# Performance work log

Hardware: AMD Instinct MI355X
Metric: run time of the kernel (lower is better)

Reference implementation:

```python
import jax, jax.numpy as jnp
import numpy as np

M, K, N = 4096, 4096, 11008  # tokens, in_features, out_features


def setup_inputs() -> dict:
    key = jax.random.key(0)
    k1, k2, k3, k4 = jax.random.split(key, 4)
    x = jax.random.normal(k1, (M, K), dtype=jnp.float32)
    weight = jax.random.randint(k2, (N, K), -128, 128).astype(jnp.int8)
    # per-output-channel scale, small positive values as from real quantization
    weight_scale = (jax.random.uniform(k3, (N,), dtype=jnp.float32) * 0.01 + 1e-4)
    bias = jax.random.normal(k4, (N,), dtype=jnp.float32)
    return {"x": x, "weight": weight, "weight_scale": weight_scale, "bias": bias}


def reference(x, weight, weight_scale, bias):
    # Dynamic per-token symmetric quantization of activations to int8.
    x_scale = jnp.max(jnp.abs(x), axis=-1, keepdims=True) / 127.0  # [M, 1]
    x_scale = jnp.maximum(x_scale, 1e-8)
    x_q = jnp.clip(jnp.round(x / x_scale), -128, 127).astype(jnp.int8)  # [M, K]
    acc = jax.lax.dot_general(
        x_q, weight,
        dimension_numbers=(((1,), (1,)), ((), ())),
        preferred_element_type=jnp.int32,
    )
    # Dequantize: per-token activation scale * per-channel weight scale, add bias.
    out = acc.astype(jnp.float32) * x_scale * weight_scale[None, :] + bias[None, :]
    return out
```

## Files before the change

### kernel.cpp

```cpp
#include <hip/hip_runtime.h>
#include <stdint.h>

#define M_DIM 4096
#define K_DIM 4096
#define N_DIM 11008

typedef int v4i __attribute__((ext_vector_type(4)));

#define LDSP(p) ((__attribute__((address_space(3))) void*)(uintptr_t)(p))
#define GLBP(p) ((__attribute__((address_space(1))) void*)(uintptr_t)(p))

__global__ __launch_bounds__(256) void quant_rows(const float* __restrict__ x,
                                                  int8_t* __restrict__ xq,
                                                  float* __restrict__ xs_out) {
    const int row = blockIdx.x;
    const int t = threadIdx.x;
    const float4* xr = (const float4*)(x + (size_t)row * K_DIM);

    float4 v[4];
    float amax = 0.0f;
#pragma unroll
    for (int r = 0; r < 4; ++r) {
        v[r] = xr[t + r * 256];
        amax = fmaxf(amax, fmaxf(fmaxf(fabsf(v[r].x), fabsf(v[r].y)),
                                 fmaxf(fabsf(v[r].z), fabsf(v[r].w))));
    }
#pragma unroll
    for (int off = 32; off > 0; off >>= 1)
        amax = fmaxf(amax, __shfl_xor(amax, off));

    __shared__ float smax[4];
    if ((t & 63) == 0) smax[t >> 6] = amax;
    __syncthreads();
    amax = fmaxf(fmaxf(smax[0], smax[1]), fmaxf(smax[2], smax[3]));

    const float xs = fmaxf(amax / 127.0f, 1e-8f);
    if (t == 0) xs_out[row] = xs;

    int* qo = (int*)(xq + (size_t)row * K_DIM);
#pragma unroll
    for (int r = 0; r < 4; ++r) {
        int q0 = (int)rintf(v[r].x / xs);
        int q1 = (int)rintf(v[r].y / xs);
        int q2 = (int)rintf(v[r].z / xs);
        int q3 = (int)rintf(v[r].w / xs);
        q0 = min(127, max(-128, q0));
        q1 = min(127, max(-128, q1));
        q2 = min(127, max(-128, q2));
        q3 = min(127, max(-128, q3));
        int packed = (q0 & 255) | ((q1 & 255) << 8) | ((q2 & 255) << 16) | (q3 << 24);
        qo[t + r * 256] = packed;
    }
}

__global__ __launch_bounds__(256) void prep_weight(const void* __restrict__ wraw,
                                                   int8_t* __restrict__ w8) {
    const int* wi = (const int*)wraw;
    int c = 0;
#pragma unroll
    for (int i = 0; i < 64; ++i) {
        int w = wi[i];
        c += (w >= -128 && w <= 127) ? 1 : 0;
    }
    const size_t tid = (size_t)blockIdx.x * 256 + threadIdx.x;
    if (c >= 32) {
        union { int4 v; char b[16]; } o;
#pragma unroll
        for (int g = 0; g < 4; ++g) {
            int4 w = ((const int4*)wraw)[tid * 4 + g];
            o.b[g * 4 + 0] = (char)w.x;
            o.b[g * 4 + 1] = (char)w.y;
            o.b[g * 4 + 2] = (char)w.z;
            o.b[g * 4 + 3] = (char)w.w;
        }
        ((int4*)w8)[tid] = o.v;
    } else {
        ((int4*)w8)[tid] = ((const int4*)wraw)[tid];
    }
}

__global__ __launch_bounds__(512, 2) void w8a8_gemm(const int8_t* __restrict__ xq,
                                                    const float* __restrict__ xscale,
                                                    const int8_t* __restrict__ wgt,
                                                    const float* __restrict__ wscale,
                                                    const float* __restrict__ bias,
                                                    float* __restrict__ out) {
    __shared__ __align__(16) int8_t lds_a[3][32768];
    __shared__ __align__(16) int8_t lds_b[2][32768];

    const int t = threadIdx.x;
    const int lane = t & 63;
    const int wave = t >> 6;
    const int wm = wave >> 2;
    const int wn = wave & 3;
    const int quad = lane >> 4;
    const int l15 = lane & 15;

    const int wg = blockIdx.x;
    const int xcd = wg & 7;
    const int u = wg >> 3;
    const int bm = 2 * xcd + (u & 1);
    const int bn = u >> 1;

    const int8_t* pa = xq + (size_t)bm * 256 * K_DIM;
    const int8_t* pb = wgt + (size_t)bn * 256 * K_DIM;

    const int srow = t >> 3;
    const size_t soff = (size_t)srow * K_DIM + (size_t)(((t & 7) ^ (srow & 7)) << 4);
    const size_t g64 = (size_t)64 * K_DIM;

#define STAGE_TILE(gb, lb)                                                                   \
    do {                                                                                     \
        __builtin_amdgcn_global_load_lds(GLBP((gb) + soff), LDSP((lb) + t * 16), 16, 0, 0);  \
        __builtin_amdgcn_global_load_lds(GLBP((gb) + soff + g64), LDSP((lb) + 8192 + t * 16), 16, 0, 0); \
        __builtin_amdgcn_global_load_lds(GLBP((gb) + soff + 2 * g64), LDSP((lb) + 16384 + t * 16), 16, 0, 0); \
        __builtin_amdgcn_global_load_lds(GLBP((gb) + soff + 3 * g64), LDSP((lb) + 24576 + t * 16), 16, 0, 0); \
    } while (0)

    int abase[2], bbase[2];
#pragma unroll
    for (int ks = 0; ks < 2; ++ks) {
        const int ar = wm * 128 + l15;
        abase[ks] = ar * 128 + (((ks * 4 + quad) ^ (l15 & 7)) << 4);
        const int br = wn * 64 + l15;
        bbase[ks] = br * 128 + (((ks * 4 + quad) ^ (l15 & 7)) << 4);
    }

    v4i acc[8][4] = {};
    v4i af[8], bf[8];

#define READ_B8(SB)                                                   \
    _Pragma("unroll") for (int j = 0; j < 4; ++j) {                   \
        bf[j] = *(const v4i*)(&lds_b[SB][bbase[0] + j * 2048]);       \
        bf[4 + j] = *(const v4i*)(&lds_b[SB][bbase[1] + j * 2048]);   \
    }
#define READ_A8(SA, KS)                                               \
    _Pragma("unroll") for (int i = 0; i < 8; ++i)                     \
        af[i] = *(const v4i*)(&lds_a[SA][abase[KS] + i * 2048]);
#define MFMA16(B0)                                                    \
    _Pragma("unroll") for (int i = 0; i < 8; ++i)                     \
    _Pragma("unroll") for (int j = 0; j < 4; ++j)                     \
        acc[i][j] = __builtin_amdgcn_mfma_i32_16x16x64_i8(            \
            af[i], bf[(B0) + j], acc[i][j], 0, 0, 0);
#define PH_PRE                                                        \
    __builtin_amdgcn_s_barrier();                                     \
    asm volatile("s_waitcnt lgkmcnt(0)" ::: "memory");                \
    __builtin_amdgcn_s_setprio(1);
#define PH_POST                                                       \
    __builtin_amdgcn_s_setprio(0);                                    \
    __builtin_amdgcn_s_barrier();

    STAGE_TILE(pa, &lds_a[0][0]);
    STAGE_TILE(pb, &lds_b[0][0]);
    STAGE_TILE(pa + 128, &lds_a[1][0]);
    STAGE_TILE(pb + 128, &lds_b[1][0]);
    asm volatile("s_waitcnt vmcnt(8)" ::: "memory");
    __builtin_amdgcn_s_barrier();

#define DO_TILE(U)                                                       \
    {                                                                    \
        constexpr int SA = (U) % 3;                                      \
        constexpr int SB = (U) % 2;                                      \
        constexpr int SA2 = ((U) + 2) % 3;                               \
        const size_t k2 = (size_t)(t0 + (U) + 2) * 128;                  \
                                                                \
        READ_B8(SB);                                                     \
        READ_A8(SA, 0);                                                  \
        STAGE_TILE(pa + k2, &lds_a[SA2][0]);                             \
        PH_PRE; MFMA16(0); PH_POST;                                      \
                                                                \
        READ_A8(SA, 1);                                                  \
        STAGE_TILE(pb + k2, &lds_b[SB][0]);                              \
        asm volatile("s_waitcnt vmcnt(8)" ::: "memory");                 \
        PH_PRE; MFMA16(4); PH_POST;                                      \
    }

#pragma unroll 1
    for (int t0 = 0; t0 < 30; t0 += 6) {
        DO_TILE(0)
        DO_TILE(1)
        DO_TILE(2)
        DO_TILE(3)
        DO_TILE(4)
        DO_TILE(5)
    }
    READ_B8(0);
    READ_A8(0, 0);
    PH_PRE; MFMA16(0); PH_POST;
    READ_A8(0, 1);
    asm volatile("s_waitcnt vmcnt(0)" ::: "memory");
    PH_PRE; MFMA16(4); PH_POST;
    READ_B8(1);
    READ_A8(1, 0);
    PH_PRE; MFMA16(0); PH_POST;
    READ_A8(1, 1);
    PH_PRE; MFMA16(4); PH_POST;

    float wsc[4], bi[4];
#pragma unroll
    for (int j = 0; j < 4; ++j) {
        const int cc = bn * 256 + wn * 64 + j * 16 + l15;
        wsc[j] = wscale[cc];
        bi[j] = bias[cc];
    }
#pragma unroll
    for (int i = 0; i < 8; ++i) {
        const int m0 = bm * 256 + wm * 128 + i * 16 + quad * 4;
        const float4 xs4 = *(const float4*)(xscale + m0);
        const float xsv[4] = {xs4.x, xs4.y, xs4.z, xs4.w};
#pragma unroll
        for (int r = 0; r < 4; ++r) {
            const size_t off = (size_t)(m0 + r) * N_DIM + (size_t)bn * 256 + wn * 64 + l15;
#pragma unroll
            for (int j = 0; j < 4; ++j) {
                out[off + j * 16] = (float)acc[i][j][r] * xsv[r] * wsc[j] + bi[j];
            }
        }
    }
}

extern "C" void kernel_launch(void* const* d_in, const int* in_sizes, int n_in,
                              void* d_out, int out_size, void* d_ws, size_t ws_size,
                              hipStream_t stream) {
    const float* x = (const float*)d_in[0];
    const void* wraw = (const void*)d_in[1];
    const float* wscale = (const float*)d_in[2];
    const float* bias = (const float*)d_in[3];
    float* out = (float*)d_out;

    int8_t* w8 = (int8_t*)d_ws;
    int8_t* xq = (int8_t*)d_ws + (size_t)N_DIM * K_DIM;
    float* xs = (float*)((char*)d_ws + (size_t)N_DIM * K_DIM + (size_t)M_DIM * K_DIM);

    quant_rows<<<M_DIM, 256, 0, stream>>>(x, xq, xs);
    prep_weight<<<(N_DIM * (K_DIM / 16)) / 256, 256, 0, stream>>>(wraw, w8);
    w8a8_gemm<<<688, 512, 0, stream>>>(xq, xs, w8, wscale, bias, out);
}
```

Baseline: 494.6 us.

## Software-pipeline LDS fragment reads with MFMA via ping-pong A register buffers

Replaces the barrier-separated read-then-compute phases with a ping-pong scheme. A fragments are split into two 4-row register sets, so the LDS reads for the next quarter are issued while MFMAs run on the current quarter. The per-half barriers go away, leaving one barrier per tile before the B restage, and the first fragments of the next tile are prefetched. The aim is to hide LDS latency and cut barrier stalls. The cost is more complex wait and ordering logic, which could introduce LDS read/write hazards.

```diff
diff --git a/kernel.cpp b/kernel.cpp
--- a/kernel.cpp
+++ b/kernel.cpp
@@ -127,28 +127,24 @@
     }
 
     v4i acc[8][4] = {};
-    v4i af[8], bf[8];
-
-#define READ_B8(SB)                                                   \
-    _Pragma("unroll") for (int j = 0; j < 4; ++j) {                   \
-        bf[j] = *(const v4i*)(&lds_b[SB][bbase[0] + j * 2048]);       \
-        bf[4 + j] = *(const v4i*)(&lds_b[SB][bbase[1] + j * 2048]);   \
-    }
-#define READ_A8(SA, KS)                                               \
-    _Pragma("unroll") for (int i = 0; i < 8; ++i)                     \
-        af[i] = *(const v4i*)(&lds_a[SA][abase[KS] + i * 2048]);
-#define MFMA16(B0)                                                    \
-    _Pragma("unroll") for (int i = 0; i < 8; ++i)                     \
+    v4i afA[4], afB[4], bf[8];
+
+#define READ_B4(SB, KS, B0)                                           \
     _Pragma("unroll") for (int j = 0; j < 4; ++j)                     \
-        acc[i][j] = __builtin_amdgcn_mfma_i32_16x16x64_i8(            \
-            af[i], bf[(B0) + j], acc[i][j], 0, 0, 0);
-#define PH_PRE                                                        \
-    __builtin_amdgcn_s_barrier();                                     \
+        bf[(B0) + j] = *(const v4i*)(&lds_b[SB][bbase[KS] + j * 2048]);
+#define READ_AQ(DST, SA, KS, I0)                                      \
+    _Pragma("unroll") for (int i = 0; i < 4; ++i)                     \
+        DST[i] = *(const v4i*)(&lds_a[SA][abase[KS] + ((I0) + i) * 2048]);
+#define MFMA4(AF, B0, R0)                                             \
+    __builtin_amdgcn_s_setprio(1);                                    \
+    _Pragma("unroll") for (int i = 0; i < 4; ++i)                     \
+    _Pragma("unroll") for (int j = 0; j < 4; ++j)                     \
+        acc[(R0) + i][j] = __builtin_amdgcn_mfma_i32_16x16x64_i8(     \
+            AF[i], bf[(B0) + j], acc[(R0) + i][j], 0, 0, 0);          \
+    __builtin_amdgcn_s_setprio(0);
+#define LGKM0                                                         \
     asm volatile("s_waitcnt lgkmcnt(0)" ::: "memory");                \
-    __builtin_amdgcn_s_setprio(1);
-#define PH_POST                                                       \
-    __builtin_amdgcn_s_setprio(0);                                    \
-    __builtin_amdgcn_s_barrier();
+    __builtin_amdgcn_sched_barrier(0);
 
     STAGE_TILE(pa, &lds_a[0][0]);
     STAGE_TILE(pb, &lds_b[0][0]);
@@ -156,23 +152,37 @@
     STAGE_TILE(pb + 128, &lds_b[1][0]);
     asm volatile("s_waitcnt vmcnt(8)" ::: "memory");
     __builtin_amdgcn_s_barrier();
+    READ_B4(0, 0, 0);
+    READ_B4(0, 1, 4);
+    READ_AQ(afA, 0, 0, 0);
+    LGKM0;
 
 #define DO_TILE(U)                                                       \
     {                                                                    \
         constexpr int SA = (U) % 3;                                      \
         constexpr int SB = (U) % 2;                                      \
+        constexpr int SA1 = ((U) + 1) % 3;                               \
+        constexpr int SB1 = ((U) + 1) % 2;                               \
         constexpr int SA2 = ((U) + 2) % 3;                               \
         const size_t k2 = (size_t)(t0 + (U) + 2) * 128;                  \
-                                                                \
-        READ_B8(SB);                                                     \
-        READ_A8(SA, 0);                                                  \
         STAGE_TILE(pa + k2, &lds_a[SA2][0]);                             \
-        PH_PRE; MFMA16(0); PH_POST;                                      \
-                                                                \
-        READ_A8(SA, 1);                                                  \
+        READ_AQ(afB, SA, 0, 4);                                          \
+        MFMA4(afA, 0, 0);                                                \
+        LGKM0;                                                           \
+        READ_AQ(afA, SA, 1, 0);                                          \
+        MFMA4(afB, 0, 4);                                                \
+        LGKM0;                                                           \
+        READ_AQ(afB, SA, 1, 4);                                          \
+        MFMA4(afA, 4, 0);                                                \
+        LGKM0;                                                           \
+        asm volatile("s_waitcnt vmcnt(4)" ::: "memory");                 \
+        __builtin_amdgcn_s_barrier();                                    \
         STAGE_TILE(pb + k2, &lds_b[SB][0]);                              \
-        asm volatile("s_waitcnt vmcnt(8)" ::: "memory");                 \
-        PH_PRE; MFMA16(4); PH_POST;                                      \
+        READ_B4(SB1, 0, 0);                                              \
+        READ_AQ(afA, SA1, 0, 0);                                         \
+        MFMA4(afB, 4, 4);                                                \
+        READ_B4(SB1, 1, 4);                                              \
+        LGKM0;                                                           \
     }
 
 #pragma unroll 1
@@ -184,17 +194,32 @@
         DO_TILE(4)
         DO_TILE(5)
     }
-    READ_B8(0);
-    READ_A8(0, 0);
-    PH_PRE; MFMA16(0); PH_POST;
-    READ_A8(0, 1);
+    READ_AQ(afB, 0, 0, 4);
+    MFMA4(afA, 0, 0);
+    LGKM0;
+    READ_AQ(afA, 0, 1, 0);
+    MFMA4(afB, 0, 4);
+    LGKM0;
+    READ_AQ(afB, 0, 1, 4);
+    MFMA4(afA, 4, 0);
+    LGKM0;
     asm volatile("s_waitcnt vmcnt(0)" ::: "memory");
-    PH_PRE; MFMA16(4); PH_POST;
-    READ_B8(1);
-    READ_A8(1, 0);
-    PH_PRE; MFMA16(0); PH_POST;
-    READ_A8(1, 1);
-    PH_PRE; MFMA16(4); PH_POST;
+    __builtin_amdgcn_s_barrier();
+    READ_B4(1, 0, 0);
+    READ_AQ(afA, 1, 0, 0);
+    MFMA4(afB, 4, 4);
+    READ_B4(1, 1, 4);
+    LGKM0;
+    READ_AQ(afB, 1, 0, 4);
+    MFMA4(afA, 0, 0);
+    LGKM0;
+    READ_AQ(afA, 1, 1, 0);
+    MFMA4(afB, 0, 4);
+    LGKM0;
+    READ_AQ(afB, 1, 1, 4);
+    MFMA4(afA, 4, 0);
+    LGKM0;
+    MFMA4(afB, 4, 4);
 
     float wsc[4], bi[4];
 #pragma unroll
```

Measured after the change: 490.4 us. About the same (-0.8%).
